# Performance work log

Hardware: AMD Instinct MI355X
Metric: run time of the kernel (lower is better)

The kernel has to match this reference:

```python
import jax, jax.numpy as jnp
import numpy as np

N_HEAD = 16

def setup_inputs() -> dict:
    key = jax.random.key(0)
    ks = jax.random.split(key, 5)
    B, T, C = 2, 2048, 1024
    s = 1.0 / np.sqrt(C)
    return {
        "x":  jax.random.normal(ks[0], (B, T, C), jnp.float32),
        "Wk": jax.random.normal(ks[1], (C, C), jnp.float32) * s,
        "Wq": jax.random.normal(ks[2], (C, C), jnp.float32) * s,
        "Wv": jax.random.normal(ks[3], (C, C), jnp.float32) * s,
        "Wp": jax.random.normal(ks[4], (C, C), jnp.float32) * s,
    }

def reference(x, Wk, Wq, Wv, Wp):
    B, T, C = x.shape
    H = N_HEAD
    D = C // H
    # torch Linear (bias=False): y = x @ W.T
    def proj(W):
        return (x @ W.T).reshape(B, T, H, D).transpose(0, 2, 1, 3)  # [B,H,T,D]
    q, k, v = proj(Wq), proj(Wk), proj(Wv)
    att = jnp.einsum("bhtd,bhsd->bhts", q, k) / jnp.sqrt(jnp.float32(D))
    causal = jnp.tril(jnp.ones((T, T), dtype=bool))
    att = jnp.where(causal[None, None], att, -jnp.inf)
    att = jax.nn.softmax(att, axis=-1)
    y = jnp.einsum("bhts,bhsd->bhtd", att, v)
    y = y.transpose(0, 2, 1, 3).reshape(B, T, C)
    return y @ Wp.T
```

## Files before the change

kernel.cpp:

```cpp
#include <hip/hip_runtime.h>

typedef unsigned short u16;
typedef unsigned int u32;
typedef unsigned long long u64;
typedef __attribute__((ext_vector_type(8))) short bf16x8;
typedef __attribute__((ext_vector_type(8))) _Float16 f16x8;
typedef __attribute__((ext_vector_type(4))) float f32x4;

#define GLOAD16(gp, lp) __builtin_amdgcn_global_load_lds( \
  (const __attribute__((address_space(1))) unsigned int*)(gp), \
  (__attribute__((address_space(3))) unsigned int*)(lp), 16, 0, 0)

__device__ __forceinline__ u16 f2bf(float f) {
  unsigned int u = __builtin_bit_cast(unsigned int, f);
  u += 0x7fffu + ((u >> 16) & 1u);
  return (u16)(u >> 16);
}

__device__ __forceinline__ u32 pk2(float a, float b) {
  return (u32)f2bf(a) | ((u32)f2bf(b) << 16);
}

__device__ __forceinline__ u32 pkh(float a, float b) {
  return __builtin_bit_cast(u32, __builtin_amdgcn_cvt_pkrtz(a, b));
}

__device__ __forceinline__ void wait_barrier() {
  asm volatile("s_waitcnt vmcnt(0)" ::: "memory");
  __builtin_amdgcn_s_barrier();
  __builtin_amdgcn_sched_barrier(0);
}

__global__ __launch_bounds__(256) void cvt_all(
    const float* __restrict__ x,
    const float* __restrict__ w0, const float* __restrict__ w1,
    const float* __restrict__ w2, const float* __restrict__ w3,
    u16* __restrict__ ox, u16* __restrict__ o0, u16* __restrict__ o1,
    u16* __restrict__ o2, u16* __restrict__ o3) {
  int bid = blockIdx.x;
  const float* in; u16* out; size_t off;
  if (bid < 4096) {
    in = x; out = ox; off = (size_t)bid << 10;
  } else {
    int r = bid - 4096, z = r >> 10;
    in  = (z == 0) ? w0 : (z == 1) ? w1 : (z == 2) ? w2 : w3;
    out = (z == 0) ? o0 : (z == 1) ? o1 : (z == 2) ? o2 : o3;
    off = (size_t)(r & 1023) << 10;
  }
  size_t i = off + (size_t)threadIdx.x * 4;
  float4 f = *reinterpret_cast<const float4*>(in + i);
  u64 v = (u64)pk2(f.x, f.y) | ((u64)pk2(f.z, f.w) << 32);
  *reinterpret_cast<u64*>(out + i) = v;
}

template<int MODE, int MI>
__device__ __forceinline__ void gemm_bt_body(
    const u16* __restrict__ A, const u16* __restrict__ Bw, void* __restrict__ Cout,
    int m0, int n0, float scale) {
  const int K = 1024;
  __shared__ __align__(16) u16 As[2][MI * 32 * 32];
  __shared__ __align__(16) u16 Bs[2][128 * 32];
  const int tid = threadIdx.x;
  const int lane = tid & 63, wid = tid >> 6;
  const int wr = wid >> 1, wc = wid & 1;
  const int g = lane >> 4, c = lane & 15;
  f32x4 acc[MI][4] = {};

  auto stage = [&](int buf, int k0) {
#pragma unroll
    for (int i = 0; i < MI / 2; ++i) {
      int idx = tid + i * 256;
      int row = idx >> 2, slot = idx & 3;
      int ss = slot ^ (row & 3);
      GLOAD16(A + (size_t)(m0 + row) * K + k0 + ss * 8, &As[buf][idx * 8]);
    }
#pragma unroll
    for (int i = 0; i < 2; ++i) {
      int idx = tid + i * 256;
      int row = idx >> 2, slot = idx & 3;
      int ss = slot ^ (row & 3);
      GLOAD16(Bw + (size_t)(n0 + row) * K + k0 + ss * 8, &Bs[buf][idx * 8]);
    }
  };

  stage(0, 0);
  int buf = 0;
#pragma unroll 1
  for (int kt = 0; kt < 32; ++kt) {
    wait_barrier();
    if (kt + 1 < 32) stage(buf ^ 1, (kt + 1) * 32);
    bf16x8 af[MI], bfr[4];
#pragma unroll
    for (int mi = 0; mi < MI; ++mi) {
      int row = wr * (MI * 16) + mi * 16 + c;
      int slot = g ^ (row & 3);
      af[mi] = *(const bf16x8*)&As[buf][row * 32 + slot * 8];
    }
#pragma unroll
    for (int ni = 0; ni < 4; ++ni) {
      int row = wc * 64 + ni * 16 + c;
      int slot = g ^ (row & 3);
      bfr[ni] = *(const bf16x8*)&Bs[buf][row * 32 + slot * 8];
    }
    __builtin_amdgcn_s_setprio(1);
#pragma unroll
    for (int mi = 0; mi < MI; ++mi)
#pragma unroll
      for (int ni = 0; ni < 4; ++ni)
        acc[mi][ni] = __builtin_amdgcn_mfma_f32_16x16x32_bf16(af[mi], bfr[ni], acc[mi][ni], 0, 0, 0);
    __builtin_amdgcn_s_setprio(0);
    buf ^= 1;
  }

#pragma unroll
  for (int mi = 0; mi < MI; ++mi)
#pragma unroll
    for (int ni = 0; ni < 4; ++ni)
#pragma unroll
      for (int i = 0; i < 4; ++i) {
        int m = m0 + wr * (MI * 16) + mi * 16 + g * 4 + i;
        int n = n0 + wc * 64 + ni * 16 + c;
        float v = acc[mi][ni][i];
        if (MODE == 0) {
          int b = m >> 11, t = m & 2047, h = n >> 6, d = n & 63;
          ((u16*)Cout)[(((size_t)b * 16 + h) * 2048 + t) * 64 + d] = f2bf(v * scale);
        } else {
          ((float*)Cout)[(size_t)m * 1024 + n] = v;
        }
      }
}

#define QSCALE 0.1803368801111204f

__global__ __launch_bounds__(256, 3) void proj_qkv(
    const u16* __restrict__ xb, const u16* __restrict__ wq, const u16* __restrict__ wk,
    const u16* __restrict__ wv, u16* __restrict__ q, u16* __restrict__ k, u16* __restrict__ v) {
  int z = blockIdx.z;
  const u16* W = (z == 0) ? wq : (z == 1) ? wk : wv;
  u16* O = (z == 0) ? q : (z == 1) ? k : v;
  float scale = (z == 0) ? QSCALE : 1.0f;
  gemm_bt_body<0, 4>(xb, W, O, blockIdx.y * 128, blockIdx.x * 128, scale);
}

__global__ __launch_bounds__(256, 2) void gemm_out(
    const u16* __restrict__ y, const u16* __restrict__ wp, float* __restrict__ out) {
  gemm_bt_body<1, 2>(y, wp, out, blockIdx.y * 64, blockIdx.x * 128, 1.0f);
}

__global__ __launch_bounds__(256) void transpose_v_kernel(
    const u16* __restrict__ v, u16* __restrict__ vt) {
  __shared__ u16 tile[64][65];
  int bh = blockIdx.y, t0 = blockIdx.x * 64;
  const u16* src = v + ((size_t)bh * 2048 + t0) * 64;
  u16* dst = vt + (size_t)bh * 64 * 2048 + t0;
  int tid = threadIdx.x;
#pragma unroll
  for (int i = 0; i < 16; ++i) {
    int idx = tid + i * 256;
    tile[idx >> 6][idx & 63] = src[idx];
  }
  __syncthreads();
#pragma unroll
  for (int i = 0; i < 16; ++i) {
    int idx = tid + i * 256;
    int d = idx >> 6, j = idx & 63;
    int t = ((j & 3) << 4) | (j >> 2);
    float f = __builtin_bit_cast(float, (u32)tile[t][d] << 16);
    _Float16 hh = (_Float16)f;
    dst[(size_t)d * 2048 + j] = __builtin_bit_cast(u16, hh);
  }
}

__global__ __launch_bounds__(256, 4) void attn_kernel(
    const u16* __restrict__ q, const u16* __restrict__ kg,
    const u16* __restrict__ vt, u16* __restrict__ y) {
  const int T = 2048;
  __shared__ __align__(16) u16 Ks[2][64 * 64];
  __shared__ __align__(16) u16 Vs[2][64 * 64];
  __shared__ __align__(16) u16 Ps[4][16 * 64];
  const int tid = threadIdx.x, lane = tid & 63, w = tid >> 6;
  const int g = lane >> 4, c = lane & 15;
  const int bh = blockIdx.x;
  const int qt = 31 - (int)blockIdx.y;
  const u16* Q = q + (size_t)bh * T * 64;
  const u16* K = kg + (size_t)bh * T * 64;
  const u16* V = vt + (size_t)bh * 64 * T;
  const int b = bh >> 4, h = bh & 15;
  const int qrow0 = qt * 64 + w * 16;

  f16x8 ones;
#pragma unroll
  for (int j = 0; j < 8; ++j) ones[j] = (_Float16)1.0f;

  auto stage = [&](int bb, int j0) {
#pragma unroll
    for (int i = 0; i < 2; ++i) {
      int idx = tid + i * 256;
      int row = idx >> 3, slot = idx & 7;
      int ss = slot ^ (row & 7);
      GLOAD16(K + (size_t)(j0 + row) * 64 + ss * 8, &Ks[bb][idx * 8]);
      GLOAD16(V + (size_t)row * T + j0 + ss * 8, &Vs[bb][idx * 8]);
    }
  };

  bf16x8 qf[2];
#pragma unroll
  for (int kk = 0; kk < 2; ++kk)
    qf[kk] = *(const bf16x8*)&Q[(size_t)(qrow0 + c) * 64 + kk * 32 + g * 8];

  f32x4 o[4] = {};
  f32x4 ol = {};

  const int nkt = qt + 1;
  stage(0, 0);
  int buf = 0;
#pragma unroll 1
  for (int kt = 0; kt < nkt; ++kt) {
    const int j0 = kt * 64;
    wait_barrier();
    if (kt + 1 < nkt) stage(buf ^ 1, j0 + 64);

    bf16x8 kb[4][2];
#pragma unroll
    for (int ni = 0; ni < 4; ++ni)
#pragma unroll
      for (int kk = 0; kk < 2; ++kk) {
        int kr = ni * 16 + c;
        int slot = (kk * 4 + g) ^ (kr & 7);
        kb[ni][kk] = *(const bf16x8*)&Ks[buf][kr * 64 + slot * 8];
      }
    f32x4 s[4];
    __builtin_amdgcn_s_setprio(1);
#pragma unroll
    for (int ni = 0; ni < 4; ++ni) {
      f32x4 a = {0.f, 0.f, 0.f, 0.f};
      a = __builtin_amdgcn_mfma_f32_16x16x32_bf16(qf[0], kb[ni][0], a, 0, 0, 0);
      a = __builtin_amdgcn_mfma_f32_16x16x32_bf16(qf[1], kb[ni][1], a, 0, 0, 0);
      s[ni] = a;
    }
    __builtin_amdgcn_s_setprio(0);

    const bool dumask = (kt == qt);
#pragma unroll
    for (int ni = 0; ni < 4; ++ni)
#pragma unroll
      for (int i = 0; i < 4; ++i) {
        float val = s[ni][i];
        if (dumask) {
          int row = qrow0 + g * 4 + i;
          int col = j0 + ni * 16 + c;
          if (col > row) val = -3.0e38f;
        }
        s[ni][i] = __builtin_amdgcn_exp2f(val);
      }

#pragma unroll
    for (int i = 0; i < 4; ++i) {
      int r = g * 4 + i;
      int slot = (c >> 1) ^ (r & 7);
      u64 val = (u64)pkh(s[0][i], s[1][i]) | ((u64)pkh(s[2][i], s[3][i]) << 32);
      *(u64*)((char*)&Ps[w][0] + r * 128 + slot * 16 + (c & 1) * 8) = val;
    }

    f16x8 pa[2], vb[4][2];
#pragma unroll
    for (int kk = 0; kk < 2; ++kk) {
      int slot = (kk * 4 + g) ^ (c & 7);
      pa[kk] = *(const f16x8*)&Ps[w][c * 64 + slot * 8];
    }
#pragma unroll
    for (int di = 0; di < 4; ++di)
#pragma unroll
      for (int kk = 0; kk < 2; ++kk) {
        int d = di * 16 + c;
        int slot = (kk * 4 + g) ^ (d & 7);
        vb[di][kk] = *(const f16x8*)&Vs[buf][d * 64 + slot * 8];
      }
    __builtin_amdgcn_s_setprio(1);
    ol = __builtin_amdgcn_mfma_f32_16x16x32_f16(pa[0], ones, ol, 0, 0, 0);
    ol = __builtin_amdgcn_mfma_f32_16x16x32_f16(pa[1], ones, ol, 0, 0, 0);
#pragma unroll
    for (int di = 0; di < 4; ++di) {
      o[di] = __builtin_amdgcn_mfma_f32_16x16x32_f16(pa[0], vb[di][0], o[di], 0, 0, 0);
      o[di] = __builtin_amdgcn_mfma_f32_16x16x32_f16(pa[1], vb[di][1], o[di], 0, 0, 0);
    }
    __builtin_amdgcn_s_setprio(0);
    buf ^= 1;
  }

#pragma unroll
  for (int i = 0; i < 4; ++i) {
    float inv = 1.f / ol[i];
    int t = qrow0 + g * 4 + i;
#pragma unroll
    for (int di = 0; di < 4; ++di) {
      int col = h * 64 + di * 16 + c;
      y[((size_t)b * 2048 + t) * 1024 + col] = f2bf(o[di][i] * inv);
    }
  }
}

extern "C" void kernel_launch(void* const* d_in, const int* in_sizes, int n_in,
                              void* d_out, int out_size, void* d_ws, size_t ws_size,
                              hipStream_t stream) {
  const float* x  = (const float*)d_in[0];
  const float* Wk = (const float*)d_in[1];
  const float* Wq = (const float*)d_in[2];
  const float* Wv = (const float*)d_in[3];
  const float* Wp = (const float*)d_in[4];
  float* out = (float*)d_out;

  char* ws = (char*)d_ws;
  const size_t SZ_X = (size_t)4096 * 1024 * 2;
  const size_t SZ_W = (size_t)1024 * 1024 * 2;
  u16* xb  = (u16*)(ws);
  u16* qb  = (u16*)(ws + SZ_X);
  u16* kb  = (u16*)(ws + 2 * SZ_X);
  u16* vb  = (u16*)(ws + 3 * SZ_X);
  u16* wqb = (u16*)(ws + 4 * SZ_X);
  u16* wkb = (u16*)(ws + 4 * SZ_X + SZ_W);
  u16* wvb = (u16*)(ws + 4 * SZ_X + 2 * SZ_W);
  u16* wpb = (u16*)(ws + 4 * SZ_X + 3 * SZ_W);

  cvt_all<<<8192, 256, 0, stream>>>(x, Wq, Wk, Wv, Wp, xb, wqb, wkb, wvb, wpb);

  proj_qkv<<<dim3(8, 32, 3), 256, 0, stream>>>(xb, wqb, wkb, wvb, qb, kb, vb);

  u16* vtb = xb;
  transpose_v_kernel<<<dim3(32, 32), 256, 0, stream>>>(vb, vtb);

  u16* yb = vb;
  attn_kernel<<<dim3(32, 32), 256, 0, stream>>>(qb, kb, vtb, yb);

  gemm_out<<<dim3(8, 64), 256, 0, stream>>>(yb, wpb, out);
}
```

Before: 112.4 us.

## Keep softmax P in registers via transposed QK^T MFMA and reorder query tiles

Swaps the MFMA operand order so S is computed transposed, which lets each lane pack its P values straight into the A-operand layout of the PV MFMA. The per-wave LDS round trip for P (write, then read back) is removed. To make this work, the V transpose kernel permutes the key order to match the new register layout, and the causal mask uses the transposed indexing. The query-tile schedule also changes from reversed order to an interleaved mix of short and long tiles, meant to balance causal work across blocks; the permutations must line up exactly for the result to stay correct.

```diff
diff --git a/kernel.cpp b/kernel.cpp
--- a/kernel.cpp
+++ b/kernel.cpp
@@ -6,6 +6,7 @@
 typedef __attribute__((ext_vector_type(8))) short bf16x8;
 typedef __attribute__((ext_vector_type(8))) _Float16 f16x8;
 typedef __attribute__((ext_vector_type(4))) float f32x4;
+typedef __attribute__((ext_vector_type(4))) u32 u32x4;
 
 #define GLOAD16(gp, lp) __builtin_amdgcn_global_load_lds( \
   (const __attribute__((address_space(1))) unsigned int*)(gp), \
@@ -164,7 +165,7 @@
   for (int i = 0; i < 16; ++i) {
     int idx = tid + i * 256;
     int d = idx >> 6, j = idx & 63;
-    int t = ((j & 3) << 4) | (j >> 2);
+    int t = (((((j >> 2) & 1) << 1) | (j >> 5)) << 4) | (((j >> 3) & 3) << 2) | (j & 3);
     float f = __builtin_bit_cast(float, (u32)tile[t][d] << 16);
     _Float16 hh = (_Float16)f;
     dst[(size_t)d * 2048 + j] = __builtin_bit_cast(u16, hh);
@@ -177,11 +178,11 @@
   const int T = 2048;
   __shared__ __align__(16) u16 Ks[2][64 * 64];
   __shared__ __align__(16) u16 Vs[2][64 * 64];
-  __shared__ __align__(16) u16 Ps[4][16 * 64];
   const int tid = threadIdx.x, lane = tid & 63, w = tid >> 6;
   const int g = lane >> 4, c = lane & 15;
   const int bh = blockIdx.x;
-  const int qt = 31 - (int)blockIdx.y;
+  const int yy = blockIdx.y, m8 = yy >> 3, o8 = yy & 7;
+  const int qt = (m8 == 0) ? o8 : (m8 == 1) ? 31 - o8 : (m8 == 2) ? 8 + o8 : 23 - o8;
   const u16* Q = q + (size_t)bh * T * 64;
   const u16* K = kg + (size_t)bh * T * 64;
   const u16* V = vt + (size_t)bh * 64 * T;
@@ -234,8 +235,8 @@
 #pragma unroll
     for (int ni = 0; ni < 4; ++ni) {
       f32x4 a = {0.f, 0.f, 0.f, 0.f};
-      a = __builtin_amdgcn_mfma_f32_16x16x32_bf16(qf[0], kb[ni][0], a, 0, 0, 0);
-      a = __builtin_amdgcn_mfma_f32_16x16x32_bf16(qf[1], kb[ni][1], a, 0, 0, 0);
+      a = __builtin_amdgcn_mfma_f32_16x16x32_bf16(kb[ni][0], qf[0], a, 0, 0, 0);
+      a = __builtin_amdgcn_mfma_f32_16x16x32_bf16(kb[ni][1], qf[1], a, 0, 0, 0);
       s[ni] = a;
     }
     __builtin_amdgcn_s_setprio(0);
@@ -247,27 +248,21 @@
       for (int i = 0; i < 4; ++i) {
         float val = s[ni][i];
         if (dumask) {
-          int row = qrow0 + g * 4 + i;
-          int col = j0 + ni * 16 + c;
-          if (col > row) val = -3.0e38f;
+          int key = j0 + ni * 16 + g * 4 + i;
+          if (key > qrow0 + c) val = -3.0e38f;
         }
         s[ni][i] = __builtin_amdgcn_exp2f(val);
       }
 
-#pragma unroll
-    for (int i = 0; i < 4; ++i) {
-      int r = g * 4 + i;
-      int slot = (c >> 1) ^ (r & 7);
-      u64 val = (u64)pkh(s[0][i], s[1][i]) | ((u64)pkh(s[2][i], s[3][i]) << 32);
-      *(u64*)((char*)&Ps[w][0] + r * 128 + slot * 16 + (c & 1) * 8) = val;
-    }
-
-    f16x8 pa[2], vb[4][2];
-#pragma unroll
-    for (int kk = 0; kk < 2; ++kk) {
-      int slot = (kk * 4 + g) ^ (c & 7);
-      pa[kk] = *(const f16x8*)&Ps[w][c * 64 + slot * 8];
-    }
+    u32x4 pa0 = { pkh(s[0][0], s[0][1]), pkh(s[0][2], s[0][3]),
+                  pkh(s[2][0], s[2][1]), pkh(s[2][2], s[2][3]) };
+    u32x4 pa1 = { pkh(s[1][0], s[1][1]), pkh(s[1][2], s[1][3]),
+                  pkh(s[3][0], s[3][1]), pkh(s[3][2], s[3][3]) };
+    f16x8 pa[2];
+    pa[0] = __builtin_bit_cast(f16x8, pa0);
+    pa[1] = __builtin_bit_cast(f16x8, pa1);
+
+    f16x8 vb[4][2];
 #pragma unroll
     for (int di = 0; di < 4; ++di)
 #pragma unroll
```

New measurement: 110.7 us (median of 2 runs). Within noise of the previous version (-1.5%).
